# Kernel tuning notes

Measured on AMD Instinct MI355X. Metric: run time of the kernel, lower is better.

The kernel has to match this reference:

```python
import jax, jax.numpy as jnp
import numpy as np

B, S, D = 4, 1024, 1024
DH = D // 8  # q/k projection dim


def setup_inputs() -> dict:
    key = jax.random.key(0)
    ks = jax.random.split(key, 16)
    std = 0.02
    inp = {
        "drums": jax.random.normal(ks[0], (B, S, D), jnp.float32),
        "vocals": jax.random.normal(ks[1], (B, S, D), jnp.float32),
        "bass": jax.random.normal(ks[2], (B, S, D), jnp.float32),
        "other": jax.random.normal(ks[3], (B, S, D), jnp.float32),
        # Linear weights stored [in, out] (transposed vs torch's [out, in])
        "DqW": jax.random.normal(ks[4], (D, DH), jnp.float32) * std,
        "Dqb": jax.random.normal(ks[5], (DH,), jnp.float32) * std,
        "DkW": jax.random.normal(ks[6], (D, DH), jnp.float32) * std,
        "Dkb": jax.random.normal(ks[7], (DH,), jnp.float32) * std,
        "DvW": jax.random.normal(ks[8], (D, D), jnp.float32) * std,
        "Dvb": jax.random.normal(ks[9], (D,), jnp.float32) * std,
        "VqW": jax.random.normal(ks[10], (D, DH), jnp.float32) * std,
        "Vqb": jax.random.normal(ks[11], (DH,), jnp.float32) * std,
        "VkW": jax.random.normal(ks[12], (D, DH), jnp.float32) * std,
        "Vkb": jax.random.normal(ks[13], (DH,), jnp.float32) * std,
        "VvW": jax.random.normal(ks[14], (D, D), jnp.float32) * std,
        "Vvb": jax.random.normal(ks[15], (D,), jnp.float32) * std,
    }
    return inp


def reference(drums, vocals, bass, other,
              DqW, Dqb, DkW, Dkb, DvW, Dvb,
              VqW, Vqb, VkW, Vkb, VvW, Vvb):
    d_model = drums.shape[-1]
    lin = lambda x, W, b: jnp.einsum("bsd,de->bse", x, W) + b
    # drums uses D_* projections; vocals/bass/other all use V_* (faithful to source)
    q = jnp.concatenate([lin(drums, DqW, Dqb), lin(vocals, VqW, Vqb),
                         lin(bass, VqW, Vqb), lin(other, VqW, Vqb)], axis=-2)
    k = jnp.concatenate([lin(drums, DkW, Dkb), lin(vocals, VkW, Vkb),
                         lin(bass, VkW, Vkb), lin(other, VkW, Vkb)], axis=-2)
    v = jnp.concatenate([lin(drums, DvW, Dvb), lin(vocals, VvW, Vvb),
                         lin(bass, VvW, Vvb), lin(other, VvW, Vvb)], axis=-2)
    # scores: [B, 4S, 4S]; dropout is identity at inference
    scores = jnp.einsum("bqe,bke->bqk", q, k) / jnp.sqrt(jnp.asarray(d_model, q.dtype))
    attn = jax.nn.softmax(scores, axis=-1)
    out = jnp.einsum("bqk,bkd->bqd", attn, v)  # [B, 4S, D]
    return out.mean(axis=-2)  # [B, D]
```

## Files before the change

### kernel.cpp

```cpp
#include <hip/hip_runtime.h>
#include <hip/hip_bf16.h>

typedef __bf16 bf16x8 __attribute__((ext_vector_type(8)));
typedef __bf16 bf16x4 __attribute__((ext_vector_type(4)));
typedef float  f32x4  __attribute__((ext_vector_type(4)));

#define MFMA(a, b, c) __builtin_amdgcn_mfma_f32_16x16x32_bf16((a), (b), (c), 0, 0, 0)

static constexpr float SC_L2E = 0.03125f * 1.44269504088896341f;
static constexpr float INV_NQ = 1.0f / 4096.0f;

__global__ __launch_bounds__(256) void kT(const float* __restrict__ Dq, const float* __restrict__ Vq,
                                          const float* __restrict__ Dk, const float* __restrict__ Vk,
                                          __bf16* __restrict__ Wt) {
    __shared__ float tile[64][65];
    int bx = blockIdx.x;
    int m = bx >> 5, rt = (bx >> 1) & 15, ct = bx & 1;
    const float* W = (m == 0) ? Dq : (m == 1) ? Vq : (m == 2) ? Dk : Vk;
    int t = threadIdx.x;
    int tr = t >> 6, tc = t & 63;
#pragma unroll
    for (int i = 0; i < 16; i++) {
        int rl = tr + i * 4;
        tile[rl][tc] = W[(size_t)(rt * 64 + rl) * 128 + ct * 64 + tc];
    }
    __syncthreads();
#pragma unroll
    for (int i = 0; i < 16; i++) {
        int cl = tr + i * 4;
        Wt[(size_t)m * 131072 + (size_t)(ct * 64 + cl) * 1024 + rt * 64 + tc] = (__bf16)tile[tc][cl];
    }
}

__global__ __launch_bounds__(256, 4) void kProj2(
    const float* __restrict__ drums, const float* __restrict__ vocals,
    const float* __restrict__ bass,  const float* __restrict__ other,
    const float* __restrict__ Dqb, const float* __restrict__ Vqb,
    const float* __restrict__ Dkb, const float* __restrict__ Vkb,
    const __bf16* __restrict__ Wt, __bf16* __restrict__ Qb, __bf16* __restrict__ Kb) {
    __shared__ uint4 xt4[128];
    char* xt = (char*)xt4;
    int bx = blockIdx.x;
    int rt = bx & 63, bs = bx >> 6;
    int b = bs >> 2, stem = bs & 3;
    int rin = rt * 16;

    const float* X = (stem == 0) ? drums : (stem == 1) ? vocals : (stem == 2) ? bass : other;
    const __bf16* WQ = Wt + (size_t)((stem == 0) ? 0 : 1) * 131072;
    const __bf16* WK = Wt + (size_t)((stem == 0) ? 2 : 3) * 131072;

    int t = threadIdx.x, lane = t & 63, wid = t >> 6;
    int l16 = lane & 15, g = lane >> 4;

    const __bf16* Wm   = (wid < 2) ? WQ : WK;
    const float*  bias = (wid < 2) ? ((stem == 0) ? Dqb : Vqb) : ((stem == 0) ? Dkb : Vkb);
    __bf16*       Out  = (wid < 2) ? Qb : Kb;
    int colbase = (wid & 1) * 64;

    int srow = t >> 4, sc4 = t & 15;
    const float* xsrc = X + ((size_t)b * 1024 + rin + srow) * 1024 + sc4 * 4;
    int swz = (srow & 7) << 4;
    char* wrp = xt + srow * 128;
    int wb = sc4 * 8;

    const __bf16* wp = Wm + (size_t)(colbase + l16) * 1024;

    f32x4 stg = *(const f32x4*)xsrc;
    bf16x8 bcur[4], bnxt[4];
#pragma unroll
    for (int cf = 0; cf < 4; cf++) bcur[cf] = *(const bf16x8*)(wp + cf * 16384 + g * 8);

    f32x4 acc[4];
#pragma unroll
    for (int cf = 0; cf < 4; cf++) acc[cf] = (f32x4){0.f, 0.f, 0.f, 0.f};

    for (int s = 0; s < 16; ++s) {
        if (s) __syncthreads();
        bf16x4 c;
        c[0] = (__bf16)stg[0]; c[1] = (__bf16)stg[1];
        c[2] = (__bf16)stg[2]; c[3] = (__bf16)stg[3];
        *(bf16x4*)(wrp + (wb ^ swz)) = c;
        __syncthreads();
        if (s < 15) stg = *(const f32x4*)(xsrc + (s + 1) * 64);
#pragma unroll
        for (int kk = 0; kk < 2; ++kk) {
            if (kk == 0 || s < 15) {
                int knk = (kk == 0) ? s * 64 + 32 : (s + 1) * 64;
#pragma unroll
                for (int cf = 0; cf < 4; cf++)
                    bnxt[cf] = *(const bf16x8*)(wp + cf * 16384 + knk + g * 8);
            }
            bf16x8 av = *(const bf16x8*)(xt + l16 * 128 + ((kk * 64 + g * 16) ^ ((l16 & 7) << 4)));
#pragma unroll
            for (int cf = 0; cf < 4; cf++) acc[cf] = MFMA(av, bcur[cf], acc[cf]);
#pragma unroll
            for (int cf = 0; cf < 4; cf++) bcur[cf] = bnxt[cf];
        }
    }

    size_t grow = (size_t)b * 4096 + (size_t)stem * 1024 + rin;
#pragma unroll
    for (int cf = 0; cf < 4; cf++) {
        int col = colbase + cf * 16 + l16;
        float bv = bias[col];
#pragma unroll
        for (int i = 0; i < 4; i++)
            Out[(grow + g * 4 + i) * 128 + col] = (__bf16)(acc[cf][i] + bv);
    }
}

__global__ __launch_bounds__(256) void kRowSum(const __bf16* __restrict__ Qb,
                                               const __bf16* __restrict__ Kb,
                                               float* __restrict__ lsum) {
    __shared__ uint4 ktile[1024];
    int bx = blockIdx.x;
    int cc = bx & 15, tile = (bx >> 4) & 31, b = bx >> 9;
    int lane = threadIdx.x & 63, wid = threadIdx.x >> 6;
    int l16 = lane & 15, g = lane >> 4;
    int R  = tile * 128 + wid * 32;
    int C0 = cc * 256;
    const __bf16* Qr = Qb + (size_t)b * 4096 * 128;
    const __bf16* Kr = Kb + (size_t)b * 4096 * 128;

    bf16x8 a[2][4];
#pragma unroll
    for (int rf = 0; rf < 2; rf++)
#pragma unroll
        for (int kf = 0; kf < 4; kf++)
            a[rf][kf] = *(const bf16x8*)(Qr + (size_t)(R + rf * 16 + l16) * 128 + kf * 32 + g * 8);

    int sr = threadIdx.x >> 2, sseg = threadIdx.x & 3;
    char* kbc = (char*)ktile;
    int swm = (sr & 7) << 4;

    uint4 st[4];
    {
        const char* src = (const char*)(Kr + (size_t)(C0 + sr) * 128) + sseg * 64;
#pragma unroll
        for (int j = 0; j < 4; j++) st[j] = *(const uint4*)(src + j * 16);
    }

    float rs[2][4] = {};
    for (int s = 0; s < 4; ++s) {
        __syncthreads();
#pragma unroll
        for (int j = 0; j < 4; j++)
            *(uint4*)(kbc + sr * 256 + ((sseg * 64 + j * 16) ^ swm)) = st[j];
        __syncthreads();
        if (s < 3) {
            const char* src = (const char*)(Kr + (size_t)(C0 + (s + 1) * 64 + sr) * 128) + sseg * 64;
#pragma unroll
            for (int j = 0; j < 4; j++) st[j] = *(const uint4*)(src + j * 16);
        }
#pragma unroll
        for (int ctl = 0; ctl < 4; ++ctl) {
            int r2 = ctl * 16 + l16;
            int rm = (r2 & 7) << 4;
            f32x4 acc0 = (f32x4){0.f,0.f,0.f,0.f};
            f32x4 acc1 = (f32x4){0.f,0.f,0.f,0.f};
#pragma unroll
            for (int kf = 0; kf < 4; kf++) {
                bf16x8 bv = *(const bf16x8*)(kbc + r2 * 256 + ((kf * 64 + g * 16) ^ rm));
                acc0 = MFMA(a[0][kf], bv, acc0);
                acc1 = MFMA(a[1][kf], bv, acc1);
            }
#pragma unroll
            for (int r = 0; r < 4; r++) {
                rs[0][r] += exp2f(acc0[r] * SC_L2E);
                rs[1][r] += exp2f(acc1[r] * SC_L2E);
            }
        }
    }
#pragma unroll
    for (int rf = 0; rf < 2; rf++)
#pragma unroll
        for (int r = 0; r < 4; r++) {
            float v = rs[rf][r];
#pragma unroll
            for (int m = 1; m < 16; m <<= 1) v += __shfl_xor(v, m);
            if (l16 == 0) atomicAdd(&lsum[(size_t)b * 4096 + R + rf * 16 + g * 4 + r], v);
        }
}

__global__ __launch_bounds__(256) void kInv(const float* __restrict__ lsum, float* __restrict__ linv) {
    int i = (blockIdx.x * 256 + threadIdx.x) * 4;
    f32x4 v = *(const f32x4*)(lsum + i);
    f32x4 r = (f32x4){1.f / v[0], 1.f / v[1], 1.f / v[2], 1.f / v[3]};
    *(f32x4*)(linv + i) = r;
}

__global__ __launch_bounds__(256) void kColSum(const __bf16* __restrict__ Qb,
                                               const __bf16* __restrict__ Kb,
                                               const float* __restrict__ linv,
                                               float* __restrict__ wsum) {
    __shared__ uint4 qtile[1024];
    __shared__ float li[256];
    int bx = blockIdx.x;
    int rc = bx & 15, tile = (bx >> 4) & 31, b = bx >> 9;
    int lane = threadIdx.x & 63, wid = threadIdx.x >> 6;
    int l16 = lane & 15, g = lane >> 4;
    int C  = tile * 128 + wid * 32;
    int R0 = rc * 256;
    const __bf16* Qr = Qb + (size_t)b * 4096 * 128;
    const __bf16* Kr = Kb + (size_t)b * 4096 * 128;

    if (threadIdx.x < 64)
        *(f32x4*)(li + threadIdx.x * 4) = *(const f32x4*)(linv + (size_t)b * 4096 + R0 + threadIdx.x * 4);

    bf16x8 kb[2][4];
#pragma unroll
    for (int cf = 0; cf < 2; cf++)
#pragma unroll
        for (int kf = 0; kf < 4; kf++)
            kb[cf][kf] = *(const bf16x8*)(Kr + (size_t)(C + cf * 16 + l16) * 128 + kf * 32 + g * 8);

    int sr = threadIdx.x >> 2, sseg = threadIdx.x & 3;
    char* qbc = (char*)qtile;
    int swm = (sr & 7) << 4;

    uint4 st[4];
    {
        const char* src = (const char*)(Qr + (size_t)(R0 + sr) * 128) + sseg * 64;
#pragma unroll
        for (int j = 0; j < 4; j++) st[j] = *(const uint4*)(src + j * 16);
    }

    float cs[2] = {0.f, 0.f};
    for (int s = 0; s < 4; ++s) {
        __syncthreads();
#pragma unroll
        for (int j = 0; j < 4; j++)
            *(uint4*)(qbc + sr * 256 + ((sseg * 64 + j * 16) ^ swm)) = st[j];
        __syncthreads();
        if (s < 3) {
            const char* src = (const char*)(Qr + (size_t)(R0 + (s + 1) * 64 + sr) * 128) + sseg * 64;
#pragma unroll
            for (int j = 0; j < 4; j++) st[j] = *(const uint4*)(src + j * 16);
        }
#pragma unroll
        for (int ctl = 0; ctl < 4; ++ctl) {
            int r2 = ctl * 16 + l16;
            int rm = (r2 & 7) << 4;
            f32x4 acc0 = (f32x4){0.f,0.f,0.f,0.f};
            f32x4 acc1 = (f32x4){0.f,0.f,0.f,0.f};
#pragma unroll
            for (int kf = 0; kf < 4; kf++) {
                bf16x8 av = *(const bf16x8*)(qbc + r2 * 256 + ((kf * 64 + g * 16) ^ rm));
                acc0 = MFMA(av, kb[0][kf], acc0);
                acc1 = MFMA(av, kb[1][kf], acc1);
            }
            int ib = s * 64 + ctl * 16 + g * 4;
#pragma unroll
            for (int r = 0; r < 4; r++) {
                float lv = li[ib + r];
                cs[0] += exp2f(acc0[r] * SC_L2E) * lv;
                cs[1] += exp2f(acc1[r] * SC_L2E) * lv;
            }
        }
    }
#pragma unroll
    for (int cf = 0; cf < 2; cf++) {
        float v = cs[cf];
        v += __shfl_xor(v, 16);
        v += __shfl_xor(v, 32);
        if (lane < 16) atomicAdd(&wsum[(size_t)b * 4096 + C + cf * 16 + lane], v);
    }
}

__global__ __launch_bounds__(256) void kY(
    const float* __restrict__ drums, const float* __restrict__ vocals,
    const float* __restrict__ bass,  const float* __restrict__ other,
    const float* __restrict__ wsum, float* __restrict__ y, float* __restrict__ alpha) {
    __shared__ float ws[16];
    int bx = blockIdx.x;
    int b = bx >> 8, stem = (bx >> 6) & 3, kc = bx & 63;
    const float* X = (stem == 0) ? drums : (stem == 1) ? vocals : (stem == 2) ? bass : other;
    int t = threadIdx.x;
    float wv = 0.f;
    if (t < 16) { wv = wsum[(size_t)b * 4096 + stem * 1024 + kc * 16 + t] * INV_NQ; ws[t] = wv; }
    __syncthreads();

    f32x4 acc = (f32x4){0.f, 0.f, 0.f, 0.f};
    const float* xp = X + ((size_t)b * 1024 + kc * 16) * 1024 + t * 4;
#pragma unroll 4
    for (int i = 0; i < 16; i++) {
        f32x4 xv = *(const f32x4*)(xp + (size_t)i * 1024);
        float wvi = ws[i];
        acc[0] += wvi * xv[0]; acc[1] += wvi * xv[1]; acc[2] += wvi * xv[2]; acc[3] += wvi * xv[3];
    }
    int seg = (stem == 0) ? 0 : 1;
    float* yp = y + ((size_t)b * 2 + seg) * 1024 + t * 4;
    atomicAdd(yp + 0, acc[0]); atomicAdd(yp + 1, acc[1]);
    atomicAdd(yp + 2, acc[2]); atomicAdd(yp + 3, acc[3]);

    if (t < 16) {
        float s = wv;
        s += __shfl_xor(s, 1); s += __shfl_xor(s, 2);
        s += __shfl_xor(s, 4); s += __shfl_xor(s, 8);
        if (t == 0) atomicAdd(alpha + b * 2 + seg, s);
    }
}

__global__ __launch_bounds__(256) void kFinal(
    const float* __restrict__ DvW, const float* __restrict__ Dvb,
    const float* __restrict__ VvW, const float* __restrict__ Vvb,
    const float* __restrict__ y, const float* __restrict__ alpha,
    float* __restrict__ out) {
    __shared__ float yD[32], yV[32];
    int bx = blockIdx.x;
    int b = bx >> 7, dstripe = (bx >> 5) & 3, kc = bx & 31;
    int t = threadIdx.x;
    if (t < 32) {
        yD[t] = y[((size_t)b * 2 + 0) * 1024 + kc * 32 + t];
        yV[t] = y[((size_t)b * 2 + 1) * 1024 + kc * 32 + t];
    }
    __syncthreads();

    int d = dstripe * 256 + t;
    const float* pD = DvW + (size_t)(kc * 32) * 1024 + d;
    const float* pV = VvW + (size_t)(kc * 32) * 1024 + d;
    float acc = 0.f;
#pragma unroll 4
    for (int k = 0; k < 32; k++)
        acc += yD[k] * pD[(size_t)k * 1024] + yV[k] * pV[(size_t)k * 1024];
    if (kc == 0) acc += alpha[b * 2] * Dvb[d] + alpha[b * 2 + 1] * Vvb[d];
    atomicAdd(out + (size_t)b * 1024 + d, acc);
}

extern "C" void kernel_launch(void* const* d_in, const int* in_sizes, int n_in,
                              void* d_out, int out_size, void* d_ws, size_t ws_size,
                              hipStream_t stream) {
    const float* drums  = (const float*)d_in[0];
    const float* vocals = (const float*)d_in[1];
    const float* bass   = (const float*)d_in[2];
    const float* other  = (const float*)d_in[3];
    const float* DqW = (const float*)d_in[4];
    const float* Dqb = (const float*)d_in[5];
    const float* DkW = (const float*)d_in[6];
    const float* Dkb = (const float*)d_in[7];
    const float* DvW = (const float*)d_in[8];
    const float* Dvb = (const float*)d_in[9];
    const float* VqW = (const float*)d_in[10];
    const float* Vqb = (const float*)d_in[11];
    const float* VkW = (const float*)d_in[12];
    const float* Vkb = (const float*)d_in[13];
    const float* VvW = (const float*)d_in[14];
    const float* Vvb = (const float*)d_in[15];
    float* out = (float*)d_out;

    char* ws = (char*)d_ws;
    __bf16* Qb   = (__bf16*)(ws);
    __bf16* Kb   = (__bf16*)(ws + (4u << 20));
    __bf16* Wt   = (__bf16*)(ws + (8u << 20));
    float*  lsum = (float*)(ws + (9u << 20));
    float*  wsum = (float*)(ws + (9u << 20) + (64u << 10));
    float*  y    = (float*)(ws + (9u << 20) + (128u << 10));
    float*  alph = (float*)(ws + (9u << 20) + (160u << 10));
    float*  linv = (float*)(ws + (9u << 20) + (192u << 10));

    hipMemsetAsync(lsum, 0, (160u << 10) + 32, stream);
    hipMemsetAsync(out, 0, (size_t)out_size * sizeof(float), stream);

    kT<<<128, 256, 0, stream>>>(DqW, VqW, DkW, VkW, Wt);
    kProj2<<<1024, 256, 0, stream>>>(drums, vocals, bass, other, Dqb, Vqb, Dkb, Vkb, Wt, Qb, Kb);
    kRowSum<<<2048, 256, 0, stream>>>(Qb, Kb, lsum);
    kInv<<<16, 256, 0, stream>>>(lsum, linv);
    kColSum<<<2048, 256, 0, stream>>>(Qb, Kb, linv, wsum);
    kY<<<1024, 256, 0, stream>>>(drums, vocals, bass, other, wsum, y, alph);
    kFinal<<<512, 256, 0, stream>>>(DvW, Dvb, VvW, Vvb, y, alph, out);
}
```

Before: 341.6 us.

## Pre-convert stem inputs to bf16 once and reuse in projection and kY

Adds a conversion kernel that writes all four stem inputs as bf16 to workspace. The projection kernel then stages 128-wide bf16 chunks instead of converting fp32 on the fly, which halves the number of k-stages and barriers. kY now reads the bf16 copy instead of fp32, halving its read traffic. The cost is an extra full fp32 read plus bf16 write pass and lower input precision in the kY weighted sum.

```diff
diff --git a/kernel.cpp b/kernel.cpp
--- a/kernel.cpp
+++ b/kernel.cpp
@@ -9,6 +9,13 @@
 
 static constexpr float SC_L2E = 0.03125f * 1.44269504088896341f;
 static constexpr float INV_NQ = 1.0f / 4096.0f;
+
+__device__ inline bf16x8 cvt2_bf8(f32x4 a, f32x4 b) {
+    bf16x8 r;
+    r[0] = (__bf16)a[0]; r[1] = (__bf16)a[1]; r[2] = (__bf16)a[2]; r[3] = (__bf16)a[3];
+    r[4] = (__bf16)b[0]; r[5] = (__bf16)b[1]; r[6] = (__bf16)b[2]; r[7] = (__bf16)b[3];
+    return r;
+}
 
 __global__ __launch_bounds__(256) void kT(const float* __restrict__ Dq, const float* __restrict__ Vq,
                                           const float* __restrict__ Dk, const float* __restrict__ Vk,
@@ -32,20 +39,38 @@
     }
 }
 
-__global__ __launch_bounds__(256, 4) void kProj2(
+__global__ __launch_bounds__(256) void kCvt(
     const float* __restrict__ drums, const float* __restrict__ vocals,
     const float* __restrict__ bass,  const float* __restrict__ other,
+    __bf16* __restrict__ Xb) {
+    size_t base = ((size_t)blockIdx.x * 256 + threadIdx.x) * 32;
+    int bs  = (int)(base >> 20);
+    int rem = (int)(base & 1048575);
+    int stem = bs & 3;
+    const float* X = (stem == 0) ? drums : (stem == 1) ? vocals : (stem == 2) ? bass : other;
+    const float* src = X + (size_t)(bs >> 2) * 1048576 + rem;
+    __bf16* dst = Xb + base;
+#pragma unroll
+    for (int j = 0; j < 4; j++) {
+        f32x4 a = *(const f32x4*)(src + j * 8);
+        f32x4 b = *(const f32x4*)(src + j * 8 + 4);
+        *(bf16x8*)(dst + j * 8) = cvt2_bf8(a, b);
+    }
+}
+
+__global__ __launch_bounds__(256, 4) void kProj3(
+    const __bf16* __restrict__ Xb,
     const float* __restrict__ Dqb, const float* __restrict__ Vqb,
     const float* __restrict__ Dkb, const float* __restrict__ Vkb,
     const __bf16* __restrict__ Wt, __bf16* __restrict__ Qb, __bf16* __restrict__ Kb) {
-    __shared__ uint4 xt4[128];
+    __shared__ uint4 xt4[256];
     char* xt = (char*)xt4;
     int bx = blockIdx.x;
     int rt = bx & 63, bs = bx >> 6;
     int b = bs >> 2, stem = bs & 3;
     int rin = rt * 16;
 
-    const float* X = (stem == 0) ? drums : (stem == 1) ? vocals : (stem == 2) ? bass : other;
+    const __bf16* Xs = Xb + ((size_t)bs << 20) + (size_t)rin * 1024;
     const __bf16* WQ = Wt + (size_t)((stem == 0) ? 0 : 1) * 131072;
     const __bf16* WK = Wt + (size_t)((stem == 0) ? 2 : 3) * 131072;
 
@@ -57,15 +82,15 @@
     __bf16*       Out  = (wid < 2) ? Qb : Kb;
     int colbase = (wid & 1) * 64;
 
-    int srow = t >> 4, sc4 = t & 15;
-    const float* xsrc = X + ((size_t)b * 1024 + rin + srow) * 1024 + sc4 * 4;
+    int srow = t >> 4, s16 = t & 15;
+    const __bf16* xsrc = Xs + (size_t)srow * 1024 + s16 * 8;
     int swz = (srow & 7) << 4;
-    char* wrp = xt + srow * 128;
-    int wb = sc4 * 8;
+    char* wrp = xt + srow * 256;
+    int wb = s16 * 16;
 
     const __bf16* wp = Wm + (size_t)(colbase + l16) * 1024;
 
-    f32x4 stg = *(const f32x4*)xsrc;
+    bf16x8 stg = *(const bf16x8*)xsrc;
     bf16x8 bcur[4], bnxt[4];
 #pragma unroll
     for (int cf = 0; cf < 4; cf++) bcur[cf] = *(const bf16x8*)(wp + cf * 16384 + g * 8);
@@ -74,23 +99,20 @@
 #pragma unroll
     for (int cf = 0; cf < 4; cf++) acc[cf] = (f32x4){0.f, 0.f, 0.f, 0.f};
 
-    for (int s = 0; s < 16; ++s) {
+    for (int s = 0; s < 8; ++s) {
         if (s) __syncthreads();
-        bf16x4 c;
-        c[0] = (__bf16)stg[0]; c[1] = (__bf16)stg[1];
-        c[2] = (__bf16)stg[2]; c[3] = (__bf16)stg[3];
-        *(bf16x4*)(wrp + (wb ^ swz)) = c;
-        __syncthreads();
-        if (s < 15) stg = *(const f32x4*)(xsrc + (s + 1) * 64);
-#pragma unroll
-        for (int kk = 0; kk < 2; ++kk) {
-            if (kk == 0 || s < 15) {
-                int knk = (kk == 0) ? s * 64 + 32 : (s + 1) * 64;
+        *(uint4*)(wrp + (wb ^ swz)) = *(uint4*)&stg;
+        __syncthreads();
+        if (s < 7) stg = *(const bf16x8*)(xsrc + (s + 1) * 128);
+#pragma unroll
+        for (int kk = 0; kk < 4; ++kk) {
+            int kf = s * 4 + kk;
+            if (kf < 31) {
 #pragma unroll
                 for (int cf = 0; cf < 4; cf++)
-                    bnxt[cf] = *(const bf16x8*)(wp + cf * 16384 + knk + g * 8);
-            }
-            bf16x8 av = *(const bf16x8*)(xt + l16 * 128 + ((kk * 64 + g * 16) ^ ((l16 & 7) << 4)));
+                    bnxt[cf] = *(const bf16x8*)(wp + cf * 16384 + (kf + 1) * 32 + g * 8);
+            }
+            bf16x8 av = *(const bf16x8*)(xt + l16 * 256 + ((kk * 64 + g * 16) ^ ((l16 & 7) << 4)));
 #pragma unroll
             for (int cf = 0; cf < 4; cf++) acc[cf] = MFMA(av, bcur[cf], acc[cf]);
 #pragma unroll
@@ -268,25 +290,24 @@
 }
 
 __global__ __launch_bounds__(256) void kY(
-    const float* __restrict__ drums, const float* __restrict__ vocals,
-    const float* __restrict__ bass,  const float* __restrict__ other,
+    const __bf16* __restrict__ Xb,
     const float* __restrict__ wsum, float* __restrict__ y, float* __restrict__ alpha) {
     __shared__ float ws[16];
     int bx = blockIdx.x;
     int b = bx >> 8, stem = (bx >> 6) & 3, kc = bx & 63;
-    const float* X = (stem == 0) ? drums : (stem == 1) ? vocals : (stem == 2) ? bass : other;
     int t = threadIdx.x;
     float wv = 0.f;
     if (t < 16) { wv = wsum[(size_t)b * 4096 + stem * 1024 + kc * 16 + t] * INV_NQ; ws[t] = wv; }
     __syncthreads();
 
     f32x4 acc = (f32x4){0.f, 0.f, 0.f, 0.f};
-    const float* xp = X + ((size_t)b * 1024 + kc * 16) * 1024 + t * 4;
+    const __bf16* xp = Xb + (((size_t)b * 4 + stem) << 20) + (size_t)kc * 16 * 1024 + t * 4;
 #pragma unroll 4
     for (int i = 0; i < 16; i++) {
-        f32x4 xv = *(const f32x4*)(xp + (size_t)i * 1024);
+        bf16x4 xv = *(const bf16x4*)(xp + (size_t)i * 1024);
         float wvi = ws[i];
-        acc[0] += wvi * xv[0]; acc[1] += wvi * xv[1]; acc[2] += wvi * xv[2]; acc[3] += wvi * xv[3];
+        acc[0] += wvi * (float)xv[0]; acc[1] += wvi * (float)xv[1];
+        acc[2] += wvi * (float)xv[2]; acc[3] += wvi * (float)xv[3];
     }
     int seg = (stem == 0) ? 0 : 1;
     float* yp = y + ((size_t)b * 2 + seg) * 1024 + t * 4;
@@ -357,15 +378,17 @@
     float*  y    = (float*)(ws + (9u << 20) + (128u << 10));
     float*  alph = (float*)(ws + (9u << 20) + (160u << 10));
     float*  linv = (float*)(ws + (9u << 20) + (192u << 10));
+    __bf16* Xb   = (__bf16*)(ws + (10u << 20));
 
     hipMemsetAsync(lsum, 0, (160u << 10) + 32, stream);
     hipMemsetAsync(out, 0, (size_t)out_size * sizeof(float), stream);
 
     kT<<<128, 256, 0, stream>>>(DqW, VqW, DkW, VkW, Wt);
-    kProj2<<<1024, 256, 0, stream>>>(drums, vocals, bass, other, Dqb, Vqb, Dkb, Vkb, Wt, Qb, Kb);
+    kCvt<<<2048, 256, 0, stream>>>(drums, vocals, bass, other, Xb);
+    kProj3<<<1024, 256, 0, stream>>>(Xb, Dqb, Vqb, Dkb, Vkb, Wt, Qb, Kb);
     kRowSum<<<2048, 256, 0, stream>>>(Qb, Kb, lsum);
     kInv<<<16, 256, 0, stream>>>(lsum, linv);
     kColSum<<<2048, 256, 0, stream>>>(Qb, Kb, linv, wsum);
-    kY<<<1024, 256, 0, stream>>>(drums, vocals, bass, other, wsum, y, alph);
+    kY<<<1024, 256, 0, stream>>>(Xb, wsum, y, alph);
     kFinal<<<512, 256, 0, stream>>>(DvW, Dvb, VvW, Vvb, y, alph, out);
 }
```

Result: slower. 358.9 us (+5.1%).
